# Optimization experiments

Measured on AMD Instinct MI355X. Metric: run time of the kernel, lower is better.

## Reference

```python
import jax, jax.numpy as jnp
import numpy as np

NOISE_STD = 0.1
TOP_K = 2


def setup_inputs() -> dict:
    key = jax.random.key(0)
    k_x, k_n, k_w, k_keys = jax.random.split(key, 4)
    N, D_IN, D_Q, K = 16384, 2048, 256, 64
    x = jax.random.normal(k_x, (N, D_IN), dtype=jnp.float32)
    noise = jax.random.normal(k_n, (N, K), dtype=jnp.float32)
    # Linear params (kaiming-uniform-ish scale) and xavier-uniform keys
    w_q = jax.random.normal(k_w, (D_IN, D_Q), dtype=jnp.float32) * (1.0 / np.sqrt(D_IN))
    b_q = jnp.zeros((D_Q,), dtype=jnp.float32)
    lim = np.sqrt(6.0 / (K + D_Q))
    keys = jax.random.uniform(k_keys, (K, D_Q), dtype=jnp.float32, minval=-lim, maxval=lim)
    return {"x": x, "noise": noise, "w_q": w_q, "b_q": b_q, "keys": keys}


def reference(x, noise, w_q, b_q, keys):
    # query projection: [N, D_in] @ [D_in, D_q] -> [N, D_q]
    query = x @ w_q + b_q
    d_q = query.shape[-1]
    # router logits: [N, K], scaled dot product with expert keys
    logits = (query @ keys.T) * (1.0 / jnp.sqrt(jnp.asarray(d_q, query.dtype)))
    logits = logits + noise * NOISE_STD  # training-mode gating noise
    # top-k selection + softmax over selected logits only
    top_logits, top_idx = jax.lax.top_k(logits, TOP_K)       # [N, top_k]
    top_probs = jax.nn.softmax(top_logits, axis=-1)           # [N, top_k]
    # scatter selected probs into dense [N, K] gating tensor (zeros elsewhere)
    rows = jnp.arange(logits.shape[0])[:, None]               # [N, 1]
    gating_probs = jnp.zeros_like(logits).at[rows, top_idx].set(top_probs)
    return gating_probs, top_idx
```

## Files before the change

### kernel.cpp

```cpp
#include <hip/hip_runtime.h>

#define MROWS 16384
#define KD 2048
#define NQ 256
#define NE 64
#define INV_SQRT_DQ 0.0625f
#define NOISE_STD_C 0.1f

typedef _Float16 f16x8 __attribute__((ext_vector_type(8)));
typedef float f32x4 __attribute__((ext_vector_type(4)));

__device__ inline void split8v(f32x4 a, f32x4 b, f16x8* h, f16x8* l) {
    f16x8 hh, ll;
#pragma unroll
    for (int i = 0; i < 4; ++i) {
        _Float16 s = (_Float16)a[i];
        hh[i] = s; ll[i] = (_Float16)(a[i] - (float)s);
    }
#pragma unroll
    for (int i = 0; i < 4; ++i) {
        _Float16 s = (_Float16)b[i];
        hh[4 + i] = s; ll[4 + i] = (_Float16)(b[i] - (float)s);
    }
    *h = hh; *l = ll;
}

__global__ __launch_bounds__(256) void prep_w2(
    const float* __restrict__ w, const float* __restrict__ keys,
    const float* __restrict__ bq, _Float16* __restrict__ whp,
    _Float16* __restrict__ wlp, float* __restrict__ css) {
    __shared__ double part[4][64][8];
    const int t = threadIdx.x;
    const int e = t & 63;
    const int qc = t >> 6;
    const int o = blockIdx.x;
    const float* kp = keys + (size_t)e * NQ + qc * 64;
    const float* wp = w + (size_t)o * 8 * NQ + qc * 64;
    double acc[8];
#pragma unroll
    for (int j = 0; j < 8; ++j) acc[j] = 0.0;
    for (int q = 0; q < 64; q += 4) {
        f32x4 kv = *(const f32x4*)(kp + q);
#pragma unroll
        for (int j = 0; j < 8; ++j) {
            f32x4 wv = *(const f32x4*)(wp + (size_t)j * NQ + q);
#pragma unroll
            for (int u = 0; u < 4; ++u)
                acc[j] += (double)wv[u] * (double)kv[u];
        }
    }
#pragma unroll
    for (int j = 0; j < 8; ++j) part[qc][e][j] = acc[j];
    __syncthreads();
    if (t < 64) {
        const size_t base = ((size_t)(o >> 2) * 4 + (e >> 4)) * 512 +
                            (size_t)((o & 3) * 16 + (e & 15)) * 8;
        f16x8 h, l;
#pragma unroll
        for (int j = 0; j < 8; ++j) {
            float v = (float)(part[0][e][j] + part[1][e][j] +
                              part[2][e][j] + part[3][e][j]);
            _Float16 s = (_Float16)v;
            h[j] = s;
            l[j] = (_Float16)(v - (float)s);
        }
        *(f16x8*)(whp + base) = h;
        *(f16x8*)(wlp + base) = l;
    }
    if (blockIdx.x == 0) {
        __syncthreads();
        double p = 0.0;
        const float* bp2 = bq + qc * 64;
        const float* kp2 = keys + (size_t)e * NQ + qc * 64;
        for (int q = 0; q < 64; q += 4) {
            f32x4 bv = *(const f32x4*)(bp2 + q);
            f32x4 kv = *(const f32x4*)(kp2 + q);
#pragma unroll
            for (int u = 0; u < 4; ++u)
                p += (double)bv[u] * (double)kv[u];
        }
        part[qc][e][0] = p;
        __syncthreads();
        if (t < 64)
            css[e] = (float)((part[0][e][0] + part[1][e][0] +
                              part[2][e][0] + part[3][e][0]) * 0.0625);
    }
}

__global__ __launch_bounds__(256, 2) void gemm3_fused(
    const float* __restrict__ x, const _Float16* __restrict__ whp,
    const _Float16* __restrict__ wlp, const float* __restrict__ css,
    const float* __restrict__ noise, float* __restrict__ gate,
    float* __restrict__ idxout) {
    __shared__ float comb[3 * 1040];
    __shared__ float LG[16 * 65];

    const int t = threadIdx.x;
    const int lane = t & 63;
    const int wv = t >> 6;
    const int m0 = blockIdx.x * 16;
    const int f = lane & 15;
    const int qq = lane >> 4;

    const float* xp = x + (size_t)(m0 + f) * KD + wv * 512 + qq * 8;
    const _Float16* bph = whp + (size_t)(wv * 16) * 2048 + lane * 8;
    const _Float16* bpl = wlp + (size_t)(wv * 16) * 2048 + lane * 8;

    f32x4 acc[4];
#pragma unroll
    for (int nt = 0; nt < 4; ++nt) acc[nt] = {0.f, 0.f, 0.f, 0.f};

    f32x4 xb[4][2];
    f16x8 bhS[2][4], blS[2][4];

#pragma unroll
    for (int s = 0; s < 4; ++s) {
        const f32x4* p = (const f32x4*)(xp + s * 32);
        xb[s][0] = __builtin_nontemporal_load(p);
        xb[s][1] = __builtin_nontemporal_load(p + 1);
    }
#pragma unroll
    for (int s = 0; s < 2; ++s)
#pragma unroll
        for (int nt = 0; nt < 4; ++nt) {
            bhS[s][nt] = *(const f16x8*)(bph + ((size_t)s * 4 + nt) * 512);
            blS[s][nt] = *(const f16x8*)(bpl + ((size_t)s * 4 + nt) * 512);
        }

#pragma unroll
    for (int s = 0; s < 16; ++s) {
        const int js = s & 3;
        const int c = s & 1;
        f16x8 ah, al;
        split8v(xb[js][0], xb[js][1], &ah, &al);
#pragma unroll
        for (int nt = 0; nt < 4; ++nt) {
            acc[nt] = __builtin_amdgcn_mfma_f32_16x16x32_f16(ah, bhS[c][nt], acc[nt], 0, 0, 0);
            acc[nt] = __builtin_amdgcn_mfma_f32_16x16x32_f16(ah, blS[c][nt], acc[nt], 0, 0, 0);
            acc[nt] = __builtin_amdgcn_mfma_f32_16x16x32_f16(al, bhS[c][nt], acc[nt], 0, 0, 0);
        }
        if (s < 12) {
            const f32x4* p = (const f32x4*)(xp + (s + 4) * 32);
            xb[js][0] = __builtin_nontemporal_load(p);
            xb[js][1] = __builtin_nontemporal_load(p + 1);
        }
        if (s < 14) {
#pragma unroll
            for (int nt = 0; nt < 4; ++nt) {
                bhS[c][nt] = *(const f16x8*)(bph + ((size_t)(s + 2) * 4 + nt) * 512);
                blS[c][nt] = *(const f16x8*)(bpl + ((size_t)(s + 2) * 4 + nt) * 512);
            }
        }
    }

    if (wv > 0) {
#pragma unroll
        for (int nt = 0; nt < 4; ++nt)
#pragma unroll
            for (int r = 0; r < 4; ++r)
                comb[(wv - 1) * 1040 + (nt * 4 + r) * 65 + lane] = acc[nt][r];
    }
    __syncthreads();
    if (wv == 0) {
#pragma unroll
        for (int nt = 0; nt < 4; ++nt)
#pragma unroll
            for (int r = 0; r < 4; ++r) {
                const int idx = (nt * 4 + r) * 65 + lane;
                acc[nt][r] += comb[idx];
                acc[nt][r] += comb[1040 + idx];
                acc[nt][r] += comb[2080 + idx];
            }
#pragma unroll
        for (int nt = 0; nt < 4; ++nt) {
            const int e = nt * 16 + f;
            const float cs = css[e];
#pragma unroll
            for (int r = 0; r < 4; ++r) {
                const int row = qq * 4 + r;
                LG[row * 65 + e] = acc[nt][r] * INV_SQRT_DQ + cs +
                                   NOISE_STD_C * noise[(size_t)(m0 + row) * NE + e];
            }
        }
    }
    __syncthreads();

    for (int i = 0; i < 4; ++i) {
        const int r = wv * 4 + i;
        float v = LG[r * 65 + lane];
        float v1 = v; int i1 = lane;
#pragma unroll
        for (int off = 32; off; off >>= 1) {
            float ov = __shfl_xor(v1, off);
            int oi = __shfl_xor(i1, off);
            if (ov > v1 || (ov == v1 && oi < i1)) { v1 = ov; i1 = oi; }
        }
        float v2 = (lane == i1) ? -1e30f : v;
        int i2 = lane;
#pragma unroll
        for (int off = 32; off; off >>= 1) {
            float ov = __shfl_xor(v2, off);
            int oi = __shfl_xor(i2, off);
            if (ov > v2 || (ov == v2 && oi < i2)) { v2 = ov; i2 = oi; }
        }
        float ex = expf(v2 - v1);
        float p1 = 1.0f / (1.0f + ex);
        float p2 = ex * p1;
        float g = (lane == i1) ? p1 : ((lane == i2) ? p2 : 0.0f);
        gate[(size_t)(m0 + r) * NE + lane] = g;
        if (lane == 0) {
            float2 ii = make_float2((float)i1, (float)i2);
            *(float2*)(idxout + (size_t)(m0 + r) * 2) = ii;
        }
    }
}

extern "C" void kernel_launch(void* const* d_in, const int* in_sizes, int n_in,
                              void* d_out, int out_size, void* d_ws, size_t ws_size,
                              hipStream_t stream) {
    const float* x     = (const float*)d_in[0];
    const float* noise = (const float*)d_in[1];
    const float* w_q   = (const float*)d_in[2];
    const float* b_q   = (const float*)d_in[3];
    const float* keys  = (const float*)d_in[4];
    float* out = (float*)d_out;

    char* ws = (char*)d_ws;
    _Float16* whp = (_Float16*)ws;
    _Float16* wlp = (_Float16*)(ws + (256u << 10));
    float* css    = (float*)(ws + (512u << 10));

    prep_w2<<<256, 256, 0, stream>>>(w_q, keys, b_q, whp, wlp, css);
    gemm3_fused<<<1024, 256, 0, stream>>>(x, whp, wlp, css, noise,
                                          out, out + (size_t)MROWS * NE);
}
```

Measured before the change: 236.5 us.

## Tile 64 rows per block with 8-wave split-K to reuse weight fragments

Each block now covers 64 rows instead of 16, using 512 threads. Each wave handles a K-slice and four M-tiles, so every loaded fp16 hi/lo weight fragment feeds four row tiles. That cuts weight re-reads from L2 by about 4x. The 8-way split-K partials are reduced through a large shared buffer with vectorized row-wise sums, and bias and noise are fused into that reduction. In exchange, shared memory use (136KB) and register pressure both grow, which limits residency to about one block per CU with a single wave of 256 blocks. The nontemporal hint on x loads is also dropped.

Result: faster. 228.7 us (-3.3%).

```diff
diff --git a/kernel.cpp b/kernel.cpp
--- a/kernel.cpp
+++ b/kernel.cpp
@@ -87,107 +87,118 @@
     }
 }
 
-__global__ __launch_bounds__(256, 2) void gemm3_fused(
+__global__ __launch_bounds__(512, 2) void gemm4_fused(
     const float* __restrict__ x, const _Float16* __restrict__ whp,
     const _Float16* __restrict__ wlp, const float* __restrict__ css,
     const float* __restrict__ noise, float* __restrict__ gate,
     float* __restrict__ idxout) {
-    __shared__ float comb[3 * 1040];
-    __shared__ float LG[16 * 65];
+    __shared__ __align__(16) char smem[139264];
 
     const int t = threadIdx.x;
     const int lane = t & 63;
     const int wv = t >> 6;
-    const int m0 = blockIdx.x * 16;
+    const int m0 = blockIdx.x * 64;
     const int f = lane & 15;
     const int qq = lane >> 4;
 
-    const float* xp = x + (size_t)(m0 + f) * KD + wv * 512 + qq * 8;
-    const _Float16* bph = whp + (size_t)(wv * 16) * 2048 + lane * 8;
-    const _Float16* bpl = wlp + (size_t)(wv * 16) * 2048 + lane * 8;
-
-    f32x4 acc[4];
-#pragma unroll
-    for (int nt = 0; nt < 4; ++nt) acc[nt] = {0.f, 0.f, 0.f, 0.f};
-
-    f32x4 xb[4][2];
+    const float* xp = x + (size_t)(m0 + f) * KD + wv * 256 + qq * 8;
+    const _Float16* bph = whp + (size_t)(wv * 8) * 2048 + lane * 8;
+    const _Float16* bpl = wlp + (size_t)(wv * 8) * 2048 + lane * 8;
+
+    f32x4 acc[4][4];
+#pragma unroll
+    for (int mt = 0; mt < 4; ++mt)
+#pragma unroll
+        for (int nt = 0; nt < 4; ++nt) acc[mt][nt] = {0.f, 0.f, 0.f, 0.f};
+
+    f32x4 xr[2][4][2];
     f16x8 bhS[2][4], blS[2][4];
 
 #pragma unroll
-    for (int s = 0; s < 4; ++s) {
-        const f32x4* p = (const f32x4*)(xp + s * 32);
-        xb[s][0] = __builtin_nontemporal_load(p);
-        xb[s][1] = __builtin_nontemporal_load(p + 1);
-    }
-#pragma unroll
-    for (int s = 0; s < 2; ++s)
+    for (int s = 0; s < 2; ++s) {
+#pragma unroll
+        for (int mt = 0; mt < 4; ++mt) {
+            const f32x4* p = (const f32x4*)(xp + (size_t)mt * 16 * KD + s * 32);
+            xr[s][mt][0] = p[0];
+            xr[s][mt][1] = p[1];
+        }
 #pragma unroll
         for (int nt = 0; nt < 4; ++nt) {
-            bhS[s][nt] = *(const f16x8*)(bph + ((size_t)s * 4 + nt) * 512);
-            blS[s][nt] = *(const f16x8*)(bpl + ((size_t)s * 4 + nt) * 512);
-        }
-
-#pragma unroll
-    for (int s = 0; s < 16; ++s) {
-        const int js = s & 3;
-        const int c = s & 1;
-        f16x8 ah, al;
-        split8v(xb[js][0], xb[js][1], &ah, &al);
-#pragma unroll
-        for (int nt = 0; nt < 4; ++nt) {
-            acc[nt] = __builtin_amdgcn_mfma_f32_16x16x32_f16(ah, bhS[c][nt], acc[nt], 0, 0, 0);
-            acc[nt] = __builtin_amdgcn_mfma_f32_16x16x32_f16(ah, blS[c][nt], acc[nt], 0, 0, 0);
-            acc[nt] = __builtin_amdgcn_mfma_f32_16x16x32_f16(al, bhS[c][nt], acc[nt], 0, 0, 0);
-        }
-        if (s < 12) {
-            const f32x4* p = (const f32x4*)(xp + (s + 4) * 32);
-            xb[js][0] = __builtin_nontemporal_load(p);
-            xb[js][1] = __builtin_nontemporal_load(p + 1);
-        }
-        if (s < 14) {
+            bhS[s][nt] = *(const f16x8*)(bph + (size_t)(s * 4 + nt) * 512);
+            blS[s][nt] = *(const f16x8*)(bpl + (size_t)(s * 4 + nt) * 512);
+        }
+    }
+
+#pragma unroll
+    for (int s = 0; s < 8; ++s) {
+        const int cs = s & 1;
+#pragma unroll
+        for (int mt = 0; mt < 4; ++mt) {
+            f16x8 ah, al;
+            split8v(xr[cs][mt][0], xr[cs][mt][1], &ah, &al);
+            if (s < 6) {
+                const f32x4* p = (const f32x4*)(xp + (size_t)mt * 16 * KD + (s + 2) * 32);
+                xr[cs][mt][0] = p[0];
+                xr[cs][mt][1] = p[1];
+            }
 #pragma unroll
             for (int nt = 0; nt < 4; ++nt) {
-                bhS[c][nt] = *(const f16x8*)(bph + ((size_t)(s + 2) * 4 + nt) * 512);
-                blS[c][nt] = *(const f16x8*)(bpl + ((size_t)(s + 2) * 4 + nt) * 512);
+                acc[mt][nt] = __builtin_amdgcn_mfma_f32_16x16x32_f16(ah, bhS[cs][nt], acc[mt][nt], 0, 0, 0);
+                acc[mt][nt] = __builtin_amdgcn_mfma_f32_16x16x32_f16(ah, blS[cs][nt], acc[mt][nt], 0, 0, 0);
+                acc[mt][nt] = __builtin_amdgcn_mfma_f32_16x16x32_f16(al, bhS[cs][nt], acc[mt][nt], 0, 0, 0);
             }
         }
-    }
-
-    if (wv > 0) {
+        if (s < 6) {
+#pragma unroll
+            for (int nt = 0; nt < 4; ++nt) {
+                bhS[cs][nt] = *(const f16x8*)(bph + (size_t)((s + 2) * 4 + nt) * 512);
+                blS[cs][nt] = *(const f16x8*)(bpl + (size_t)((s + 2) * 4 + nt) * 512);
+            }
+        }
+    }
+
+    float* part = (float*)smem;
+#pragma unroll
+    for (int mt = 0; mt < 4; ++mt)
 #pragma unroll
         for (int nt = 0; nt < 4; ++nt)
 #pragma unroll
             for (int r = 0; r < 4; ++r)
-                comb[(wv - 1) * 1040 + (nt * 4 + r) * 65 + lane] = acc[nt][r];
-    }
-    __syncthreads();
-    if (wv == 0) {
-#pragma unroll
-        for (int nt = 0; nt < 4; ++nt)
-#pragma unroll
-            for (int r = 0; r < 4; ++r) {
-                const int idx = (nt * 4 + r) * 65 + lane;
-                acc[nt][r] += comb[idx];
-                acc[nt][r] += comb[1040 + idx];
-                acc[nt][r] += comb[2080 + idx];
-            }
-#pragma unroll
-        for (int nt = 0; nt < 4; ++nt) {
-            const int e = nt * 16 + f;
-            const float cs = css[e];
-#pragma unroll
-            for (int r = 0; r < 4; ++r) {
-                const int row = qq * 4 + r;
-                LG[row * 65 + e] = acc[nt][r] * INV_SQRT_DQ + cs +
-                                   NOISE_STD_C * noise[(size_t)(m0 + row) * NE + e];
-            }
-        }
-    }
-    __syncthreads();
-
-    for (int i = 0; i < 4; ++i) {
-        const int r = wv * 4 + i;
-        float v = LG[r * 65 + lane];
+                part[(size_t)(wv * 64 + mt * 16 + qq * 4 + r) * 68 + nt * 16 + f] =
+                    acc[mt][nt][r];
+    __syncthreads();
+
+    const int rrow = t >> 3;
+    const int e0 = (t & 7) * 8;
+    f32x4 s0 = {0.f, 0.f, 0.f, 0.f}, s1 = {0.f, 0.f, 0.f, 0.f};
+#pragma unroll
+    for (int w = 0; w < 8; ++w) {
+        const float* pp = part + (size_t)(w * 64 + rrow) * 68 + e0;
+        f32x4 u = *(const f32x4*)pp;
+        f32x4 v = *(const f32x4*)(pp + 4);
+#pragma unroll
+        for (int j = 0; j < 4; ++j) { s0[j] += u[j]; s1[j] += v[j]; }
+    }
+    f32x4 c0 = *(const f32x4*)(css + e0);
+    f32x4 c1 = *(const f32x4*)(css + e0 + 4);
+    const float* np = noise + (size_t)(m0 + rrow) * NE + e0;
+    f32x4 n0 = *(const f32x4*)np;
+    f32x4 n1 = *(const f32x4*)(np + 4);
+#pragma unroll
+    for (int j = 0; j < 4; ++j) {
+        s0[j] = s0[j] * INV_SQRT_DQ + c0[j] + NOISE_STD_C * n0[j];
+        s1[j] = s1[j] * INV_SQRT_DQ + c1[j] + NOISE_STD_C * n1[j];
+    }
+    __syncthreads();
+
+    float* LG = (float*)smem;
+    *(f32x4*)(LG + (size_t)rrow * 68 + e0) = s0;
+    *(f32x4*)(LG + (size_t)rrow * 68 + e0 + 4) = s1;
+    __syncthreads();
+
+    for (int i = 0; i < 8; ++i) {
+        const int r = wv * 8 + i;
+        float v = LG[(size_t)r * 68 + lane];
         float v1 = v; int i1 = lane;
 #pragma unroll
         for (int off = 32; off; off >>= 1) {
@@ -231,6 +242,6 @@
     float* css    = (float*)(ws + (512u << 10));
 
     prep_w2<<<256, 256, 0, stream>>>(w_q, keys, b_q, whp, wlp, css);
-    gemm3_fused<<<1024, 256, 0, stream>>>(x, whp, wlp, css, noise,
-                                          out, out + (size_t)MROWS * NE);
-}
+    gemm4_fused<<<256, 512, 0, stream>>>(x, whp, wlp, css, noise,
+                                         out, out + (size_t)MROWS * NE);
+}
```

## Stage split x tiles in LDS with 64-row blocks and 2x4 wave tiling

Applied to the files above, without the earlier changes.

The fused GEMM now processes 64 rows per block with 8 waves arranged 2x4 over rows and experts. Each x element is converted to fp16 hi/lo only once into double-buffered, XOR-swizzled LDS, rather than each wave splitting its own K-slice. This removes the cross-wave K-split reduction and reuses each weight fragment across two M tiles. In exchange it adds a barrier per K step, uses regular loads instead of nontemporal ones, and launches only 256 blocks, which may underfill the GPU.

Measured after the change: 227.4 us. 1.04x faster.

```diff
diff --git a/kernel.cpp b/kernel.cpp
--- a/kernel.cpp
+++ b/kernel.cpp
@@ -8,19 +8,15 @@
 #define NOISE_STD_C 0.1f
 
 typedef _Float16 f16x8 __attribute__((ext_vector_type(8)));
+typedef _Float16 f16x4 __attribute__((ext_vector_type(4)));
 typedef float f32x4 __attribute__((ext_vector_type(4)));
 
-__device__ inline void split8v(f32x4 a, f32x4 b, f16x8* h, f16x8* l) {
-    f16x8 hh, ll;
+__device__ inline void split4v(f32x4 a, f16x4* h, f16x4* l) {
+    f16x4 hh, ll;
 #pragma unroll
     for (int i = 0; i < 4; ++i) {
         _Float16 s = (_Float16)a[i];
         hh[i] = s; ll[i] = (_Float16)(a[i] - (float)s);
-    }
-#pragma unroll
-    for (int i = 0; i < 4; ++i) {
-        _Float16 s = (_Float16)b[i];
-        hh[4 + i] = s; ll[4 + i] = (_Float16)(b[i] - (float)s);
     }
     *h = hh; *l = ll;
 }
@@ -87,107 +83,142 @@
     }
 }
 
-__global__ __launch_bounds__(256, 2) void gemm3_fused(
+__global__ __launch_bounds__(512) void gemm5_fused(
     const float* __restrict__ x, const _Float16* __restrict__ whp,
     const _Float16* __restrict__ wlp, const float* __restrict__ css,
     const float* __restrict__ noise, float* __restrict__ gate,
     float* __restrict__ idxout) {
-    __shared__ float comb[3 * 1040];
-    __shared__ float LG[16 * 65];
+    __shared__ __align__(16) char smem[32768];
 
     const int t = threadIdx.x;
     const int lane = t & 63;
     const int wv = t >> 6;
-    const int m0 = blockIdx.x * 16;
+    const int wn = wv & 3;
+    const int wm = wv >> 2;
+    const int m0 = blockIdx.x * 64;
     const int f = lane & 15;
     const int qq = lane >> 4;
 
-    const float* xp = x + (size_t)(m0 + f) * KD + wv * 512 + qq * 8;
-    const _Float16* bph = whp + (size_t)(wv * 16) * 2048 + lane * 8;
-    const _Float16* bpl = wlp + (size_t)(wv * 16) * 2048 + lane * 8;
-
-    f32x4 acc[4];
-#pragma unroll
-    for (int nt = 0; nt < 4; ++nt) acc[nt] = {0.f, 0.f, 0.f, 0.f};
-
-    f32x4 xb[4][2];
-    f16x8 bhS[2][4], blS[2][4];
-
+    const int sr = t >> 4;
+    const int sc = t & 15;
+    const int soct = sc >> 1;
+    const int shalf = sc & 1;
+    const float* xp0 = x + (size_t)(m0 + sr) * KD + sc * 4;
+    const float* xp1 = x + (size_t)(m0 + sr + 32) * KD + sc * 4;
+    const int wde0 = sr * 64 + ((soct ^ (sr & 7)) * 8) + shalf * 4;
+    const int wde1 = wde0 + 32 * 64;
+
+    const _Float16* bph = whp + (size_t)wn * 512 + lane * 8;
+    const _Float16* bpl = wlp + (size_t)wn * 512 + lane * 8;
+
+    f32x4 acc[2];
+    acc[0] = {0.f, 0.f, 0.f, 0.f};
+    acc[1] = {0.f, 0.f, 0.f, 0.f};
+
+    f16x8 bhS[4], blS[4];
 #pragma unroll
     for (int s = 0; s < 4; ++s) {
-        const f32x4* p = (const f32x4*)(xp + s * 32);
-        xb[s][0] = __builtin_nontemporal_load(p);
-        xb[s][1] = __builtin_nontemporal_load(p + 1);
-    }
-#pragma unroll
-    for (int s = 0; s < 2; ++s)
-#pragma unroll
-        for (int nt = 0; nt < 4; ++nt) {
-            bhS[s][nt] = *(const f16x8*)(bph + ((size_t)s * 4 + nt) * 512);
-            blS[s][nt] = *(const f16x8*)(bpl + ((size_t)s * 4 + nt) * 512);
-        }
-
-#pragma unroll
-    for (int s = 0; s < 16; ++s) {
-        const int js = s & 3;
-        const int c = s & 1;
-        f16x8 ah, al;
-        split8v(xb[js][0], xb[js][1], &ah, &al);
-#pragma unroll
-        for (int nt = 0; nt < 4; ++nt) {
-            acc[nt] = __builtin_amdgcn_mfma_f32_16x16x32_f16(ah, bhS[c][nt], acc[nt], 0, 0, 0);
-            acc[nt] = __builtin_amdgcn_mfma_f32_16x16x32_f16(ah, blS[c][nt], acc[nt], 0, 0, 0);
-            acc[nt] = __builtin_amdgcn_mfma_f32_16x16x32_f16(al, bhS[c][nt], acc[nt], 0, 0, 0);
-        }
-        if (s < 12) {
-            const f32x4* p = (const f32x4*)(xp + (s + 4) * 32);
-            xb[js][0] = __builtin_nontemporal_load(p);
-            xb[js][1] = __builtin_nontemporal_load(p + 1);
-        }
-        if (s < 14) {
-#pragma unroll
-            for (int nt = 0; nt < 4; ++nt) {
-                bhS[c][nt] = *(const f16x8*)(bph + ((size_t)(s + 2) * 4 + nt) * 512);
-                blS[c][nt] = *(const f16x8*)(bpl + ((size_t)(s + 2) * 4 + nt) * 512);
+        bhS[s] = *(const f16x8*)(bph + (size_t)s * 2048);
+        blS[s] = *(const f16x8*)(bpl + (size_t)s * 2048);
+    }
+
+    f32x4 e0, e1, o0, o1;
+    e0 = *(const f32x4*)xp0;
+    e1 = *(const f32x4*)xp1;
+    {
+        _Float16* Ah = (_Float16*)smem;
+        _Float16* Al = Ah + 4096;
+        f16x4 h, l;
+        split4v(e0, &h, &l);
+        *(f16x4*)(Ah + wde0) = h; *(f16x4*)(Al + wde0) = l;
+        split4v(e1, &h, &l);
+        *(f16x4*)(Ah + wde1) = h; *(f16x4*)(Al + wde1) = l;
+    }
+    o0 = *(const f32x4*)(xp0 + 64);
+    o1 = *(const f32x4*)(xp1 + 64);
+    e0 = *(const f32x4*)(xp0 + 128);
+    e1 = *(const f32x4*)(xp1 + 128);
+    __syncthreads();
+
+    for (int ii = 0; ii < 16; ++ii) {
+#pragma unroll
+        for (int j = 0; j < 2; ++j) {
+            const int i = ii * 2 + j;
+            _Float16* AhC = (_Float16*)smem + j * 8192;
+            _Float16* AlC = AhC + 4096;
+            _Float16* AhN = (_Float16*)smem + (j ^ 1) * 8192;
+            _Float16* AlN = AhN + 4096;
+
+            if (i < 31) {
+                f16x4 h, l;
+                if (j == 0) {
+                    split4v(o0, &h, &l);
+                    *(f16x4*)(AhN + wde0) = h; *(f16x4*)(AlN + wde0) = l;
+                    split4v(o1, &h, &l);
+                    *(f16x4*)(AhN + wde1) = h; *(f16x4*)(AlN + wde1) = l;
+                } else {
+                    split4v(e0, &h, &l);
+                    *(f16x4*)(AhN + wde0) = h; *(f16x4*)(AlN + wde0) = l;
+                    split4v(e1, &h, &l);
+                    *(f16x4*)(AhN + wde1) = h; *(f16x4*)(AlN + wde1) = l;
+                }
             }
-        }
-    }
-
-    if (wv > 0) {
-#pragma unroll
-        for (int nt = 0; nt < 4; ++nt)
-#pragma unroll
-            for (int r = 0; r < 4; ++r)
-                comb[(wv - 1) * 1040 + (nt * 4 + r) * 65 + lane] = acc[nt][r];
-    }
-    __syncthreads();
-    if (wv == 0) {
-#pragma unroll
-        for (int nt = 0; nt < 4; ++nt)
-#pragma unroll
-            for (int r = 0; r < 4; ++r) {
-                const int idx = (nt * 4 + r) * 65 + lane;
-                acc[nt][r] += comb[idx];
-                acc[nt][r] += comb[1040 + idx];
-                acc[nt][r] += comb[2080 + idx];
+            if (i < 29) {
+                if (j == 0) {
+                    o0 = *(const f32x4*)(xp0 + (i + 3) * 64);
+                    o1 = *(const f32x4*)(xp1 + (i + 3) * 64);
+                } else {
+                    e0 = *(const f32x4*)(xp0 + (i + 3) * 64);
+                    e1 = *(const f32x4*)(xp1 + (i + 3) * 64);
+                }
             }
 #pragma unroll
-        for (int nt = 0; nt < 4; ++nt) {
-            const int e = nt * 16 + f;
-            const float cs = css[e];
-#pragma unroll
-            for (int r = 0; r < 4; ++r) {
-                const int row = qq * 4 + r;
-                LG[row * 65 + e] = acc[nt][r] * INV_SQRT_DQ + cs +
-                                   NOISE_STD_C * noise[(size_t)(m0 + row) * NE + e];
+            for (int ks = 0; ks < 2; ++ks) {
+                const int slot = (2 * j + ks) & 3;
+                f16x8 ah[2], al[2];
+#pragma unroll
+                for (int mt = 0; mt < 2; ++mt) {
+                    const int row = wm * 32 + mt * 16 + f;
+                    const int off = row * 64 + (((ks * 4 + qq) ^ (f & 7)) * 8);
+                    ah[mt] = *(const f16x8*)(AhC + off);
+                    al[mt] = *(const f16x8*)(AlC + off);
+                }
+#pragma unroll
+                for (int mt = 0; mt < 2; ++mt) {
+                    acc[mt] = __builtin_amdgcn_mfma_f32_16x16x32_f16(ah[mt], bhS[slot], acc[mt], 0, 0, 0);
+                    acc[mt] = __builtin_amdgcn_mfma_f32_16x16x32_f16(ah[mt], blS[slot], acc[mt], 0, 0, 0);
+                    acc[mt] = __builtin_amdgcn_mfma_f32_16x16x32_f16(al[mt], bhS[slot], acc[mt], 0, 0, 0);
+                }
+                int gn = 2 * i + ks + 4;
+                if (gn > 63) gn = 63;
+                bhS[slot] = *(const f16x8*)(bph + (size_t)gn * 2048);
+                blS[slot] = *(const f16x8*)(bpl + (size_t)gn * 2048);
             }
-        }
-    }
-    __syncthreads();
-
-    for (int i = 0; i < 4; ++i) {
-        const int r = wv * 4 + i;
-        float v = LG[r * 65 + lane];
+            asm volatile("" ::: "memory");
+            __builtin_amdgcn_s_waitcnt(0xC07F);
+            __builtin_amdgcn_s_barrier();
+            asm volatile("" ::: "memory");
+        }
+    }
+
+    __syncthreads();
+
+    float* LG = (float*)smem;
+    const int e = wn * 16 + f;
+    const float cse = css[e];
+#pragma unroll
+    for (int mt = 0; mt < 2; ++mt)
+#pragma unroll
+        for (int r = 0; r < 4; ++r) {
+            const int row = wm * 32 + mt * 16 + qq * 4 + r;
+            LG[row * 68 + e] = acc[mt][r] * INV_SQRT_DQ + cse +
+                               NOISE_STD_C * noise[(size_t)(m0 + row) * NE + e];
+        }
+    __syncthreads();
+
+    for (int i = 0; i < 8; ++i) {
+        const int r = wv * 8 + i;
+        float v = LG[r * 68 + lane];
         float v1 = v; int i1 = lane;
 #pragma unroll
         for (int off = 32; off; off >>= 1) {
@@ -231,6 +262,6 @@
     float* css    = (float*)(ws + (512u << 10));
 
     prep_w2<<<256, 256, 0, stream>>>(w_q, keys, b_q, whp, wlp, css);
-    gemm3_fused<<<1024, 256, 0, stream>>>(x, whp, wlp, css, noise,
-                                          out, out + (size_t)MROWS * NE);
-}
+    gemm5_fused<<<256, 512, 0, stream>>>(x, whp, wlp, css, noise,
+                                         out, out + (size_t)MROWS * NE);
+}
```

## Restructure fused GEMM into 64-row tiles with async LDS DMA pipeline

Applied to the files above, without the earlier changes.

Replaces the 16-row, split-K-across-waves kernel with a 512-thread block that handles 64 rows. X and the split fp16 weight tiles are streamed into LDS through a 4-stage ring of global_load_lds transfers, using an XOR swizzle and vmcnt-based barriers. This removes the cross-wave reduction through shared memory and lets weight tiles be shared by more rows. The cost is 128KB of LDS per block, which allows only one block per CU, and a grid of 256 blocks, so occupancy and CU coverage are lower.

Measured after the change: 225.3 us. 4.7% less time.

```diff
diff --git a/kernel.cpp b/kernel.cpp
--- a/kernel.cpp
+++ b/kernel.cpp
@@ -10,7 +10,7 @@
 typedef _Float16 f16x8 __attribute__((ext_vector_type(8)));
 typedef float f32x4 __attribute__((ext_vector_type(4)));
 
-__device__ inline void split8v(f32x4 a, f32x4 b, f16x8* h, f16x8* l) {
+__device__ __forceinline__ void split8v(f32x4 a, f32x4 b, f16x8* h, f16x8* l) {
     f16x8 hh, ll;
 #pragma unroll
     for (int i = 0; i < 4; ++i) {
@@ -23,6 +23,12 @@
         hh[4 + i] = s; ll[4 + i] = (_Float16)(b[i] - (float)s);
     }
     *h = hh; *l = ll;
+}
+
+__device__ __forceinline__ void dma16(const void* g, void* l) {
+    __builtin_amdgcn_global_load_lds(
+        (const __attribute__((address_space(1))) void*)g,
+        (__attribute__((address_space(3))) void*)l, 16, 0, 0);
 }
 
 __global__ __launch_bounds__(256) void prep_w2(
@@ -87,107 +93,135 @@
     }
 }
 
-__global__ __launch_bounds__(256, 2) void gemm3_fused(
+__global__ __launch_bounds__(512) void gemm6_fused(
     const float* __restrict__ x, const _Float16* __restrict__ whp,
     const _Float16* __restrict__ wlp, const float* __restrict__ css,
     const float* __restrict__ noise, float* __restrict__ gate,
     float* __restrict__ idxout) {
-    __shared__ float comb[3 * 1040];
-    __shared__ float LG[16 * 65];
+    __shared__ __align__(16) char smem[131072];
 
     const int t = threadIdx.x;
     const int lane = t & 63;
     const int wv = t >> 6;
-    const int m0 = blockIdx.x * 16;
+    const int wn = wv & 3;
+    const int wm = wv >> 2;
+    const int m0 = blockIdx.x * 64;
     const int f = lane & 15;
     const int qq = lane >> 4;
 
-    const float* xp = x + (size_t)(m0 + f) * KD + wv * 512 + qq * 8;
-    const _Float16* bph = whp + (size_t)(wv * 16) * 2048 + lane * 8;
-    const _Float16* bpl = wlp + (size_t)(wv * 16) * 2048 + lane * 8;
-
-    f32x4 acc[4];
-#pragma unroll
-    for (int nt = 0; nt < 4; ++nt) acc[nt] = {0.f, 0.f, 0.f, 0.f};
-
-    f32x4 xb[4][2];
-    f16x8 bhS[2][4], blS[2][4];
-
-#pragma unroll
-    for (int s = 0; s < 4; ++s) {
-        const f32x4* p = (const f32x4*)(xp + s * 32);
-        xb[s][0] = __builtin_nontemporal_load(p);
-        xb[s][1] = __builtin_nontemporal_load(p + 1);
-    }
-#pragma unroll
-    for (int s = 0; s < 2; ++s)
-#pragma unroll
-        for (int nt = 0; nt < 4; ++nt) {
-            bhS[s][nt] = *(const f16x8*)(bph + ((size_t)s * 4 + nt) * 512);
-            blS[s][nt] = *(const f16x8*)(bpl + ((size_t)s * 4 + nt) * 512);
-        }
-
-#pragma unroll
-    for (int s = 0; s < 16; ++s) {
-        const int js = s & 3;
-        const int c = s & 1;
-        f16x8 ah, al;
-        split8v(xb[js][0], xb[js][1], &ah, &al);
-#pragma unroll
-        for (int nt = 0; nt < 4; ++nt) {
-            acc[nt] = __builtin_amdgcn_mfma_f32_16x16x32_f16(ah, bhS[c][nt], acc[nt], 0, 0, 0);
-            acc[nt] = __builtin_amdgcn_mfma_f32_16x16x32_f16(ah, blS[c][nt], acc[nt], 0, 0, 0);
-            acc[nt] = __builtin_amdgcn_mfma_f32_16x16x32_f16(al, bhS[c][nt], acc[nt], 0, 0, 0);
-        }
-        if (s < 12) {
-            const f32x4* p = (const f32x4*)(xp + (s + 4) * 32);
-            xb[js][0] = __builtin_nontemporal_load(p);
-            xb[js][1] = __builtin_nontemporal_load(p + 1);
-        }
-        if (s < 14) {
-#pragma unroll
-            for (int nt = 0; nt < 4; ++nt) {
-                bhS[c][nt] = *(const f16x8*)(bph + ((size_t)(s + 2) * 4 + nt) * 512);
-                blS[c][nt] = *(const f16x8*)(bpl + ((size_t)(s + 2) * 4 + nt) * 512);
-            }
-        }
-    }
-
-    if (wv > 0) {
-#pragma unroll
-        for (int nt = 0; nt < 4; ++nt)
-#pragma unroll
-            for (int r = 0; r < 4; ++r)
-                comb[(wv - 1) * 1040 + (nt * 4 + r) * 65 + lane] = acc[nt][r];
-    }
+    const int sr = t >> 4;
+    const int sc = t & 15;
+    const float* xs0 = x + (size_t)(m0 + sr) * KD + (sc ^ (sr & 15)) * 4;
+    const float* xs1 = xs0 + (size_t)32 * KD;
+    const int xdst = wv * 1024;
+    const int bdst = (wv >> 2) * 4096 + wn * 1024;
+    const char* bsh = (const char*)whp + (size_t)((wv >> 2) * 4 + wn) * 1024 + lane * 16;
+    const char* bsl = (const char*)wlp + (size_t)((wv >> 2) * 4 + wn) * 1024 + lane * 16;
+
+    const int rb0 = (wm * 32 + f) * 256;
+    const int rb1 = rb0 + 4096;
+    const int ck0 = ((qq * 2) ^ f) * 16;
+    const int ck1 = ((8 + qq * 2) ^ f) * 16;
+
+    f32x4 acc[2];
+    acc[0] = {0.f, 0.f, 0.f, 0.f};
+    acc[1] = {0.f, 0.f, 0.f, 0.f};
+
+#define ISSUE(t_, s_)                                                          \
+    do {                                                                       \
+        dma16(xs0 + (t_) * 64, smem + (s_) * 16384 + xdst);                    \
+        dma16(xs1 + (t_) * 64, smem + (s_) * 16384 + xdst + 8192);             \
+        dma16(bsh + (size_t)(t_) * 8192, smem + 65536 + (s_) * 16384 + bdst);  \
+        dma16(bsl + (size_t)(t_) * 8192,                                       \
+              smem + 65536 + (s_) * 16384 + bdst + 8192);                      \
+    } while (0)
+
+#define COMPUTE(s_)                                                            \
+    do {                                                                       \
+        const char* xb = smem + (s_) * 16384;                                  \
+        const char* bb = smem + 65536 + (s_) * 16384 + wn * 1024 + lane * 16;  \
+        f16x8 bh0 = *(const f16x8*)(bb);                                       \
+        f16x8 bl0 = *(const f16x8*)(bb + 8192);                                \
+        f16x8 bh1 = *(const f16x8*)(bb + 4096);                                \
+        f16x8 bl1 = *(const f16x8*)(bb + 4096 + 8192);                         \
+        f16x8 ah0, al0, ah1, al1;                                              \
+        {                                                                      \
+            f32x4 u0 = *(const f32x4*)(xb + rb0 + ck0);                        \
+            f32x4 v0 = *(const f32x4*)(xb + rb0 + (ck0 ^ 16));                 \
+            f32x4 u1 = *(const f32x4*)(xb + rb1 + ck0);                        \
+            f32x4 v1 = *(const f32x4*)(xb + rb1 + (ck0 ^ 16));                 \
+            split8v(u0, v0, &ah0, &al0);                                       \
+            split8v(u1, v1, &ah1, &al1);                                       \
+            acc[0] = __builtin_amdgcn_mfma_f32_16x16x32_f16(ah0, bh0, acc[0], 0, 0, 0); \
+            acc[0] = __builtin_amdgcn_mfma_f32_16x16x32_f16(ah0, bl0, acc[0], 0, 0, 0); \
+            acc[0] = __builtin_amdgcn_mfma_f32_16x16x32_f16(al0, bh0, acc[0], 0, 0, 0); \
+            acc[1] = __builtin_amdgcn_mfma_f32_16x16x32_f16(ah1, bh0, acc[1], 0, 0, 0); \
+            acc[1] = __builtin_amdgcn_mfma_f32_16x16x32_f16(ah1, bl0, acc[1], 0, 0, 0); \
+            acc[1] = __builtin_amdgcn_mfma_f32_16x16x32_f16(al1, bh0, acc[1], 0, 0, 0); \
+        }                                                                      \
+        {                                                                      \
+            f32x4 u0 = *(const f32x4*)(xb + rb0 + ck1);                        \
+            f32x4 v0 = *(const f32x4*)(xb + rb0 + (ck1 ^ 16));                 \
+            f32x4 u1 = *(const f32x4*)(xb + rb1 + ck1);                        \
+            f32x4 v1 = *(const f32x4*)(xb + rb1 + (ck1 ^ 16));                 \
+            split8v(u0, v0, &ah0, &al0);                                       \
+            split8v(u1, v1, &ah1, &al1);                                       \
+            acc[0] = __builtin_amdgcn_mfma_f32_16x16x32_f16(ah0, bh1, acc[0], 0, 0, 0); \
+            acc[0] = __builtin_amdgcn_mfma_f32_16x16x32_f16(ah0, bl1, acc[0], 0, 0, 0); \
+            acc[0] = __builtin_amdgcn_mfma_f32_16x16x32_f16(al0, bh1, acc[0], 0, 0, 0); \
+            acc[1] = __builtin_amdgcn_mfma_f32_16x16x32_f16(ah1, bh1, acc[1], 0, 0, 0); \
+            acc[1] = __builtin_amdgcn_mfma_f32_16x16x32_f16(ah1, bl1, acc[1], 0, 0, 0); \
+            acc[1] = __builtin_amdgcn_mfma_f32_16x16x32_f16(al1, bh1, acc[1], 0, 0, 0); \
+        }                                                                      \
+    } while (0)
+
+#define WAITBAR(vm_)                                                           \
+    do {                                                                       \
+        asm volatile("s_waitcnt vmcnt(" #vm_ ")" ::: "memory");                \
+        __builtin_amdgcn_s_barrier();                                          \
+        __builtin_amdgcn_sched_barrier(0);                                     \
+    } while (0)
+
+    ISSUE(0, 0);
+    ISSUE(1, 1);
+    ISSUE(2, 2);
+
+    for (int ii = 0; ii < 7; ++ii) {
+#pragma unroll
+        for (int u = 0; u < 4; ++u) {
+            const int i = ii * 4 + u;
+            WAITBAR(8);
+            ISSUE(i + 3, (u + 3) & 3);
+            COMPUTE(u);
+        }
+    }
+    WAITBAR(8); ISSUE(31, 3); COMPUTE(0);
+    WAITBAR(8); COMPUTE(1);
+    WAITBAR(4); COMPUTE(2);
+    WAITBAR(0); COMPUTE(3);
+
+#undef ISSUE
+#undef COMPUTE
+#undef WAITBAR
+
     __syncthreads();
-    if (wv == 0) {
-#pragma unroll
-        for (int nt = 0; nt < 4; ++nt)
-#pragma unroll
-            for (int r = 0; r < 4; ++r) {
-                const int idx = (nt * 4 + r) * 65 + lane;
-                acc[nt][r] += comb[idx];
-                acc[nt][r] += comb[1040 + idx];
-                acc[nt][r] += comb[2080 + idx];
-            }
-#pragma unroll
-        for (int nt = 0; nt < 4; ++nt) {
-            const int e = nt * 16 + f;
-            const float cs = css[e];
-#pragma unroll
-            for (int r = 0; r < 4; ++r) {
-                const int row = qq * 4 + r;
-                LG[row * 65 + e] = acc[nt][r] * INV_SQRT_DQ + cs +
-                                   NOISE_STD_C * noise[(size_t)(m0 + row) * NE + e];
-            }
-        }
-    }
+
+    float* LG = (float*)smem;
+    const int e = wn * 16 + f;
+    const float cse = css[e];
+#pragma unroll
+    for (int mt = 0; mt < 2; ++mt)
+#pragma unroll
+        for (int r = 0; r < 4; ++r) {
+            const int row = wm * 32 + mt * 16 + qq * 4 + r;
+            LG[row * 68 + e] = acc[mt][r] * INV_SQRT_DQ + cse +
+                               NOISE_STD_C * noise[(size_t)(m0 + row) * NE + e];
+        }
     __syncthreads();
 
-    for (int i = 0; i < 4; ++i) {
-        const int r = wv * 4 + i;
-        float v = LG[r * 65 + lane];
+    for (int i = 0; i < 8; ++i) {
+        const int r = wv * 8 + i;
+        float v = LG[r * 68 + lane];
         float v1 = v; int i1 = lane;
 #pragma unroll
         for (int off = 32; off; off >>= 1) {
@@ -209,8 +243,8 @@
         float g = (lane == i1) ? p1 : ((lane == i2) ? p2 : 0.0f);
         gate[(size_t)(m0 + r) * NE + lane] = g;
         if (lane == 0) {
-            float2 ii = make_float2((float)i1, (float)i2);
-            *(float2*)(idxout + (size_t)(m0 + r) * 2) = ii;
+            float2 ii2 = make_float2((float)i1, (float)i2);
+            *(float2*)(idxout + (size_t)(m0 + r) * 2) = ii2;
         }
     }
 }
@@ -231,6 +265,6 @@
     float* css    = (float*)(ws + (512u << 10));
 
     prep_w2<<<256, 256, 0, stream>>>(w_q, keys, b_q, whp, wlp, css);
-    gemm3_fused<<<1024, 256, 0, stream>>>(x, whp, wlp, css, noise,
-                                          out, out + (size_t)MROWS * NE);
-}
+    gemm6_fused<<<256, 512, 0, stream>>>(x, whp, wlp, css, noise,
+                                         out, out + (size_t)MROWS * NE);
+}
```
